# Kernel tuning notes

Hardware: AMD Instinct MI355X
Metric: run time of the kernel (lower is better)

The kernel has to match this reference:

```python
import jax, jax.numpy as jnp
import numpy as np

N_NODES = 50000
N_EDGES = 800000
IN_DIM = 64
OUT_DIM = 64
HID = OUT_DIM // 2  # 32
N_LAYERS = 9  # layer_num; layer_num >= 7 => no temporal conv, conv dropout unused


def _layernorm(x, w, b, eps=1e-5):
    mu = jnp.mean(x, axis=-1, keepdims=True)
    var = jnp.var(x, axis=-1, keepdims=True)
    return (x - mu) * jax.lax.rsqrt(var + eps) * w + b


def _conv(x, Wp, Wn, Ws, src, tgt, pos_m, neg_m):
    # relation-wise gather -> linear -> masked merge -> single scatter_add
    xs = x[src]  # [E, d_in]
    m = jnp.where(pos_m[:, None], xs @ Wp.T, 0.0) + jnp.where(neg_m[:, None], xs @ Wn.T, 0.0)
    agg = jax.ops.segment_sum(m, tgt, num_segments=N_NODES)
    return agg + x @ Ws.T


def _asfr(x, ln_w, ln_b, gw, gb):
    xn = _layernorm(x, ln_w, ln_b)
    w = jax.nn.sigmoid(xn @ gw.T + gb)
    w1 = jnp.where(w > 0.5, 1.0, w)
    w2 = jnp.where(w > 0.5, 0.0, w)
    x1 = w1 * x
    x2 = w2 * x
    h = x.shape[1] // 2
    return jnp.concatenate([x1[:, :h] + x2[:, h:], x1[:, h:] + x2[:, :h]], axis=1)


def setup_inputs() -> dict:
    key = jax.random.key(0)
    ks = jax.random.split(key, 24)
    init_emb = jax.random.normal(ks[0], (N_NODES, IN_DIM), dtype=jnp.float32)
    src = jax.random.randint(ks[1], (N_EDGES,), 0, N_NODES)
    tgt = jax.random.randint(ks[2], (N_EDGES,), 0, N_NODES)
    sign = jnp.where(jax.random.uniform(ks[3], (N_EDGES,)) > 0.5, 1, -1).astype(jnp.int64)
    edge_index_s = jnp.stack([src, tgt, sign], axis=1).astype(jnp.int64)

    def w(k, shape, fan_in):
        return jax.random.normal(k, shape, dtype=jnp.float32) * (1.0 / np.sqrt(fan_in))

    inp = dict(init_emb=init_emb, edge_index_s=edge_index_s)
    # conv1: in 64 -> 32, relations pos/neg + self loop (no bias)
    inp["W1_pos"] = w(ks[4], (HID, IN_DIM), IN_DIM)
    inp["W1_neg"] = w(ks[5], (HID, IN_DIM), IN_DIM)
    inp["W1_self"] = w(ks[6], (HID, IN_DIM), IN_DIM)
    # 8 further convs: 32 -> 32, stacked
    L = N_LAYERS - 1
    inp["Wl_pos"] = w(ks[7], (L, HID, HID), HID)
    inp["Wl_neg"] = w(ks[8], (L, HID, HID), HID)
    inp["Wl_self"] = w(ks[9], (L, HID, HID), HID)
    # ASFR
    inp["asfr_ln_w"] = jnp.ones((HID,), jnp.float32)
    inp["asfr_ln_b"] = jnp.zeros((HID,), jnp.float32)
    inp["asfr_gate_w"] = w(ks[10], (HID, HID), HID)
    inp["asfr_gate_b"] = jnp.zeros((HID,), jnp.float32)
    # projection 32 -> 64
    inp["proj_w"] = w(ks[11], (OUT_DIM, HID), HID)
    inp["proj_b"] = jnp.zeros((OUT_DIM,), jnp.float32)
    # readout MLP: 64 -> 64 -> 64 -> 1, layernorm + relu between
    inp["mlp_w1"] = w(ks[12], (OUT_DIM, OUT_DIM), OUT_DIM)
    inp["mlp_b1"] = jnp.zeros((OUT_DIM,), jnp.float32)
    inp["mlp_ln1_w"] = jnp.ones((OUT_DIM,), jnp.float32)
    inp["mlp_ln1_b"] = jnp.zeros((OUT_DIM,), jnp.float32)
    inp["mlp_w2"] = w(ks[13], (OUT_DIM, OUT_DIM), OUT_DIM)
    inp["mlp_b2"] = jnp.zeros((OUT_DIM,), jnp.float32)
    inp["mlp_ln2_w"] = jnp.ones((OUT_DIM,), jnp.float32)
    inp["mlp_ln2_b"] = jnp.zeros((OUT_DIM,), jnp.float32)
    inp["mlp_w3"] = w(ks[14], (1, OUT_DIM), OUT_DIM)
    inp["mlp_b3"] = jnp.zeros((1,), jnp.float32)
    return inp


def reference(init_emb, edge_index_s, W1_pos, W1_neg, W1_self, Wl_pos, Wl_neg, Wl_self,
              asfr_ln_w, asfr_ln_b, asfr_gate_w, asfr_gate_b, proj_w, proj_b,
              mlp_w1, mlp_b1, mlp_ln1_w, mlp_ln1_b, mlp_w2, mlp_b2,
              mlp_ln2_w, mlp_ln2_b, mlp_w3, mlp_b3):
    src = edge_index_s[:, 0]
    tgt = edge_index_s[:, 1]
    sign = edge_index_s[:, 2]
    pos_m = sign > 0
    neg_m = sign < 0

    z = jax.nn.elu(_conv(init_emb, W1_pos, W1_neg, W1_self, src, tgt, pos_m, neg_m))
    z = _asfr(z, asfr_ln_w, asfr_ln_b, asfr_gate_w, asfr_gate_b)
    for i in range(Wl_pos.shape[0]):
        z_new = jax.nn.elu(_conv(z, Wl_pos[i], Wl_neg[i], Wl_self[i], src, tgt, pos_m, neg_m))
        z = z_new if i == 0 else z_new + 0.1 * z
    z = jax.nn.elu(z @ proj_w.T + proj_b)
    # readout MLP (eval mode: dropout identity)
    h = jax.nn.relu(_layernorm(z @ mlp_w1.T + mlp_b1, mlp_ln1_w, mlp_ln1_b))
    h = jax.nn.relu(_layernorm(h @ mlp_w2.T + mlp_b2, mlp_ln2_w, mlp_ln2_b))
    prob = jax.nn.sigmoid(h @ mlp_w3.T + mlp_b3)
    return (z, prob)
```

## Files before the change

### kernel.cpp

```cpp
#include <hip/hip_runtime.h>
#include <hip/hip_bf16.h>

#define NODES 50000
#define EDGES 800000
#define BSH 8
#define NBUCK 196
#define NBIN_BLOCKS 391

__device__ __forceinline__ float elu1(float x) { return x > 0.f ? x : expm1f(x); }

union F4 { float4 v; float f[4]; };

__global__ __launch_bounds__(256) void k_hist2(const int* __restrict__ ei, int* __restrict__ deg,
                                               int* __restrict__ bucket_cnt) {
  __shared__ int cnt[NBUCK];
  int t = threadIdx.x;
  for (int i = t; i < NBUCK; i += 256) cnt[i] = 0;
  __syncthreads();
  int base = blockIdx.x * 2048;
#pragma unroll
  for (int i = 0; i < 8; i++) {
    int e = base + i * 256 + t;
    if (e < EDGES) {
      int tgt = ei[e * 3 + 1];
      atomicAdd(deg + tgt, 1);
      atomicAdd(&cnt[tgt >> BSH], 1);
    }
  }
  __syncthreads();
  for (int i = t; i < NBUCK; i += 256)
    if (cnt[i]) atomicAdd(bucket_cnt + i, cnt[i]);
}

__global__ __launch_bounds__(512) void k_scan1(const int* __restrict__ deg, int* __restrict__ offs,
                                               int* __restrict__ bsum) {
  __shared__ int s[512];
  int t = threadIdx.x, i = blockIdx.x * 512 + t;
  int v = (i < NODES) ? deg[i] : 0;
  s[t] = v;
  __syncthreads();
  for (int o = 1; o < 512; o <<= 1) {
    int x = (t >= o) ? s[t - o] : 0;
    __syncthreads();
    s[t] += x;
    __syncthreads();
  }
  if (i < NODES) offs[i] = s[t] - v;
  if (t == 511) bsum[blockIdx.x] = s[511];
}

__global__ __launch_bounds__(128) void k_scan2(int* __restrict__ bsum, int nb) {
  __shared__ int s[128];
  int t = threadIdx.x;
  int v = (t < nb) ? bsum[t] : 0;
  s[t] = v;
  __syncthreads();
  for (int o = 1; o < 128; o <<= 1) {
    int x = (t >= o) ? s[t - o] : 0;
    __syncthreads();
    s[t] += x;
    __syncthreads();
  }
  if (t < nb) bsum[t] = s[t] - v;
}

__global__ __launch_bounds__(512) void k_scan3(int* __restrict__ offs, const int* __restrict__ bsum) {
  int i = blockIdx.x * 512 + threadIdx.x;
  if (i < NODES) offs[i] += bsum[blockIdx.x];
  if (i == 0) offs[NODES] = EDGES;
}

__global__ __launch_bounds__(256) void k_bscan(const int* __restrict__ bucket_cnt,
                                               int* __restrict__ bucket_base,
                                               int* __restrict__ bucket_cursor) {
  __shared__ int s[256];
  int t = threadIdx.x;
  int v = (t < NBUCK) ? bucket_cnt[t] : 0;
  s[t] = v;
  __syncthreads();
  for (int o = 1; o < 256; o <<= 1) {
    int x = (t >= o) ? s[t - o] : 0;
    __syncthreads();
    s[t] += x;
    __syncthreads();
  }
  if (t < NBUCK) { int e = s[t] - v; bucket_base[t] = e; bucket_cursor[t] = e; }
}

__global__ __launch_bounds__(256) void k_bin(const int* __restrict__ ei,
                                             int* __restrict__ bucket_cursor,
                                             uint2* __restrict__ binned) {
  __shared__ int cnt[NBUCK], base[NBUCK];
  int t = threadIdx.x;
  for (int i = t; i < NBUCK; i += 256) cnt[i] = 0;
  __syncthreads();
  int eb = blockIdx.x * 2048;
#pragma unroll
  for (int i = 0; i < 8; i++) {
    int e = eb + i * 256 + t;
    if (e < EDGES) atomicAdd(&cnt[ei[e * 3 + 1] >> BSH], 1);
  }
  __syncthreads();
  for (int i = t; i < NBUCK; i += 256) {
    int c = cnt[i];
    base[i] = c ? atomicAdd(bucket_cursor + i, c) : 0;
    cnt[i] = 0;
  }
  __syncthreads();
#pragma unroll
  for (int i = 0; i < 8; i++) {
    int e = eb + i * 256 + t;
    if (e < EDGES) {
      int src = ei[e * 3 + 0];
      int tgt = ei[e * 3 + 1];
      int sg  = ei[e * 3 + 2];
      unsigned val = (unsigned)src | (sg < 0 ? 0x80000000u : 0u);
      int bkt = tgt >> BSH;
      int r = atomicAdd(&cnt[bkt], 1);
      binned[base[bkt] + r] = make_uint2(val, (unsigned)tgt);
    }
  }
}

__global__ __launch_bounds__(256) void k_scatter2(const uint2* __restrict__ binned,
                                                  const int* __restrict__ bucket_base,
                                                  const int* __restrict__ bucket_cnt,
                                                  const int* __restrict__ offs,
                                                  unsigned* __restrict__ perm) {
  __shared__ int cur[256];
  int b = blockIdx.x, t = threadIdx.x;
  int t0 = b << BSH;
  cur[t] = (t0 + t < NODES) ? offs[t0 + t] : 0;
  __syncthreads();
  int n = bucket_cnt[b], bb = bucket_base[b];
  for (int i = t; i < n; i += 256) {
    uint2 e = binned[bb + i];
    int p = atomicAdd(&cur[e.y - t0], 1);
    perm[p] = e.x;
  }
}

__global__ __launch_bounds__(256) void k_lin64(const float* __restrict__ x,
    const float* __restrict__ Wp, const float* __restrict__ Wn, const float* __restrict__ Ws,
    __hip_bfloat16* __restrict__ ypb, __hip_bfloat16* __restrict__ ynb, float* __restrict__ ys) {
  constexpr int K4 = 16;
  __shared__ float4 wp[K4][32], wn[K4][32], wsm[K4][32];
  __shared__ float4 xs[8][K4];
  for (int i = threadIdx.x; i < 32 * K4; i += 256) {
    int k4 = i >> 5, c = i & 31;
    wp[k4][c]  = ((const float4*)Wp)[c * K4 + k4];
    wn[k4][c]  = ((const float4*)Wn)[c * K4 + k4];
    wsm[k4][c] = ((const float4*)Ws)[c * K4 + k4];
  }
  int base = blockIdx.x * 8;
  for (int i = threadIdx.x; i < 8 * K4; i += 256) {
    int r = i / K4, k4 = i - r * K4;
    xs[r][k4] = ((const float4*)(x + (size_t)(base + r) * 64))[k4];
  }
  __syncthreads();
  int lane = threadIdx.x & 31, local = threadIdx.x >> 5;
  float ap = 0.f, an = 0.f, asf = 0.f;
#pragma unroll
  for (int k4 = 0; k4 < K4; k4++) {
    float4 xv = xs[local][k4];
    float4 a = wp[k4][lane], b = wn[k4][lane], c = wsm[k4][lane];
    ap  = fmaf(xv.w, a.w, fmaf(xv.z, a.z, fmaf(xv.y, a.y, fmaf(xv.x, a.x, ap))));
    an  = fmaf(xv.w, b.w, fmaf(xv.z, b.z, fmaf(xv.y, b.y, fmaf(xv.x, b.x, an))));
    asf = fmaf(xv.w, c.w, fmaf(xv.z, c.z, fmaf(xv.y, c.y, fmaf(xv.x, c.x, asf))));
  }
  size_t o = (size_t)(base + local) * 32 + lane;
  ypb[o] = __float2bfloat16(ap);
  ynb[o] = __float2bfloat16(an);
  ys[o] = asf;
}

#define ACC8(A, V)                                   \
  A[0] += __uint_as_float((V).x << 16);              \
  A[1] += __uint_as_float((V).x & 0xffff0000u);      \
  A[2] += __uint_as_float((V).y << 16);              \
  A[3] += __uint_as_float((V).y & 0xffff0000u);      \
  A[4] += __uint_as_float((V).z << 16);              \
  A[5] += __uint_as_float((V).z & 0xffff0000u);      \
  A[6] += __uint_as_float((V).w << 16);              \
  A[7] += __uint_as_float((V).w & 0xffff0000u);

template <int DO_ASFR, int DO_RES, int DO_LIN, int WRITE_Z>
__global__ __launch_bounds__(256) void k_layer(
    const unsigned short* __restrict__ ypi, const unsigned short* __restrict__ yni,
    float* __restrict__ ys,
    const unsigned* __restrict__ perm, const int* __restrict__ offs,
    float* __restrict__ z,
    const float* __restrict__ lnw, const float* __restrict__ lnb,
    const float* __restrict__ gw, const float* __restrict__ gb,
    const float* __restrict__ Wp, const float* __restrict__ Wn, const float* __restrict__ Ws,
    __hip_bfloat16* __restrict__ ypo, __hip_bfloat16* __restrict__ yno) {
  __shared__ float4 wps[8][32], wns[8][32], wss[8][32], gws[8][32];
  __shared__ float zrow[8][36], xrow[8][36];
  int t = threadIdx.x;
  if (DO_LIN) {
    int k4 = t >> 5, c = t & 31;
    wps[k4][c] = ((const float4*)Wp)[c * 8 + k4];
    wns[k4][c] = ((const float4*)Wn)[c * 8 + k4];
    wss[k4][c] = ((const float4*)Ws)[c * 8 + k4];
    if (DO_ASFR) gws[k4][c] = ((const float4*)gw)[c * 8 + k4];
  }
  int lane = t & 31, local = t >> 5;
  int node = blockIdx.x * 8 + local;
  int es = lane >> 2, fs = lane & 3;
  int beg = offs[node], end = offs[node + 1];
  float a0[8], a1[8];
#pragma unroll
  for (int i = 0; i < 8; i++) { a0[i] = 0.f; a1[i] = 0.f; }
  int b = beg + es;
  for (; b + 8 < end; b += 16) {
    unsigned u0 = perm[b];
    unsigned u1 = perm[b + 8];
    const unsigned short* p0 = (u0 >> 31) ? yni : ypi;
    const unsigned short* p1 = (u1 >> 31) ? yni : ypi;
    uint4 v0 = *((const uint4*)(p0 + (size_t)(u0 & 0x7FFFFFFFu) * 32) + fs);
    uint4 v1 = *((const uint4*)(p1 + (size_t)(u1 & 0x7FFFFFFFu) * 32) + fs);
    ACC8(a0, v0);
    ACC8(a1, v1);
  }
  if (b < end) {
    unsigned u0 = perm[b];
    const unsigned short* p0 = (u0 >> 31) ? yni : ypi;
    uint4 v0 = *((const uint4*)(p0 + (size_t)(u0 & 0x7FFFFFFFu) * 32) + fs);
    ACC8(a0, v0);
  }
#pragma unroll
  for (int i = 0; i < 8; i++) a0[i] += a1[i];
#pragma unroll
  for (int m = 4; m <= 16; m <<= 1) {
#pragma unroll
    for (int i = 0; i < 8; i++) a0[i] += __shfl_xor(a0[i], m, 32);
  }
  if (es == 0) {
    const float* ysr = ys + (size_t)node * 32 + fs * 8;
    F4 s0, s1;
    s0.v = *(const float4*)ysr;
    s1.v = *(const float4*)(ysr + 4);
    float o[8];
#pragma unroll
    for (int i = 0; i < 4; i++) o[i] = elu1(a0[i] + s0.f[i]);
#pragma unroll
    for (int i = 0; i < 4; i++) o[4 + i] = elu1(a0[4 + i] + s1.f[i]);
    if (DO_RES) {
      const float* rr = z + (size_t)node * 32 + fs * 8;
      F4 r0, r1;
      r0.v = *(const float4*)rr;
      r1.v = *(const float4*)(rr + 4);
#pragma unroll
      for (int i = 0; i < 4; i++) { o[i] += 0.1f * r0.f[i]; o[4 + i] += 0.1f * r1.f[i]; }
    }
#pragma unroll
    for (int i = 0; i < 8; i++) zrow[local][fs * 8 + i] = o[i];
    if (WRITE_Z) {
      float* zw = z + (size_t)node * 32 + fs * 8;
      *(float4*)zw = make_float4(o[0], o[1], o[2], o[3]);
      *(float4*)(zw + 4) = make_float4(o[4], o[5], o[6], o[7]);
    }
  }
  __syncthreads();
  if (!DO_LIN) return;
  if (DO_ASFR) {
    float v = zrow[local][lane];
    float s = v;
#pragma unroll
    for (int m = 16; m; m >>= 1) s += __shfl_xor(s, m, 32);
    float mu = s * (1.f / 32.f);
    float d = v - mu, sq = d * d;
#pragma unroll
    for (int m = 16; m; m >>= 1) sq += __shfl_xor(sq, m, 32);
    float xn = d * rsqrtf(sq * (1.f / 32.f) + 1e-5f) * lnw[lane] + lnb[lane];
    xrow[local][lane] = xn;
    float ga = gb[lane];
#pragma unroll
    for (int k4 = 0; k4 < 8; k4++) {
      float4 xv = *((const float4*)&xrow[local][0] + k4);
      float4 w = gws[k4][lane];
      ga = fmaf(xv.w, w.w, fmaf(xv.z, w.z, fmaf(xv.y, w.y, fmaf(xv.x, w.x, ga))));
    }
    float g = 1.f / (1.f + __expf(-ga));
    float w1 = g > 0.5f ? 1.f : g;
    float w2 = g > 0.5f ? 0.f : g;
    float zn = w1 * v + __shfl_xor(w2 * v, 16, 32);
    zrow[local][lane] = zn;
  }
  float ap = 0.f, an = 0.f, asf = 0.f;
#pragma unroll
  for (int k4 = 0; k4 < 8; k4++) {
    float4 xv = *((const float4*)&zrow[local][0] + k4);
    float4 a2 = wps[k4][lane], b2 = wns[k4][lane], c2 = wss[k4][lane];
    ap  = fmaf(xv.w, a2.w, fmaf(xv.z, a2.z, fmaf(xv.y, a2.y, fmaf(xv.x, a2.x, ap))));
    an  = fmaf(xv.w, b2.w, fmaf(xv.z, b2.z, fmaf(xv.y, b2.y, fmaf(xv.x, b2.x, an))));
    asf = fmaf(xv.w, c2.w, fmaf(xv.z, c2.z, fmaf(xv.y, c2.y, fmaf(xv.x, c2.x, asf))));
  }
  size_t o = (size_t)node * 32 + lane;
  ypo[o] = __float2bfloat16(ap);
  yno[o] = __float2bfloat16(an);
  ys[o] = asf;
}

__global__ __launch_bounds__(256) void k_mlp(const float* __restrict__ z,
    const float* __restrict__ pw, const float* __restrict__ pb,
    const float* __restrict__ w1, const float* __restrict__ b1,
    const float* __restrict__ l1w, const float* __restrict__ l1b,
    const float* __restrict__ w2, const float* __restrict__ b2,
    const float* __restrict__ l2w, const float* __restrict__ l2b,
    const float* __restrict__ w3, const float* __restrict__ b3,
    float* __restrict__ outz, float* __restrict__ outp) {
  __shared__ float4 pT4[32 * 16];
  __shared__ float4 w1T4[64 * 16], w2T4[64 * 16];
  __shared__ float4 hbuf4[64 * 17];
  __shared__ float pb_s[64], b1_s[64], l1w_s[64], l1b_s[64], b2_s[64], l2w_s[64], l2b_s[64], w3_s[64];
  int t = threadIdx.x;
  for (int i = t; i < 512; i += 256) {
    int k = i >> 4, j4 = i & 15;
    float4 v;
    v.x = pw[(j4 * 4 + 0) * 32 + k]; v.y = pw[(j4 * 4 + 1) * 32 + k];
    v.z = pw[(j4 * 4 + 2) * 32 + k]; v.w = pw[(j4 * 4 + 3) * 32 + k];
    pT4[i] = v;
  }
  for (int i = t; i < 1024; i += 256) {
    int k = i >> 4, j4 = i & 15;
    float4 v, u;
    v.x = w1[(j4 * 4 + 0) * 64 + k]; v.y = w1[(j4 * 4 + 1) * 64 + k];
    v.z = w1[(j4 * 4 + 2) * 64 + k]; v.w = w1[(j4 * 4 + 3) * 64 + k];
    u.x = w2[(j4 * 4 + 0) * 64 + k]; u.y = w2[(j4 * 4 + 1) * 64 + k];
    u.z = w2[(j4 * 4 + 2) * 64 + k]; u.w = w2[(j4 * 4 + 3) * 64 + k];
    w1T4[i] = v; w2T4[i] = u;
  }
  if (t < 64) {
    pb_s[t] = pb[t]; b1_s[t] = b1[t]; l1w_s[t] = l1w[t]; l1b_s[t] = l1b[t];
    b2_s[t] = b2[t]; l2w_s[t] = l2w[t]; l2b_s[t] = l2b[t]; w3_s[t] = w3[t];
  }
  __syncthreads();
  int g = t >> 2, q = t & 3;
  int node = blockIdx.x * 64 + g;
  if (node >= NODES) return;
  float bb3 = b3[0];
  {
    const float4* z4 = (const float4*)(z + (size_t)node * 32);
    hbuf4[g * 17 + q * 2 + 0] = z4[q * 2 + 0];
    hbuf4[g * 17 + q * 2 + 1] = z4[q * 2 + 1];
  }
  float acc[16], h[16];
#pragma unroll
  for (int i = 0; i < 16; i++) acc[i] = pb_s[q * 16 + i];
#pragma unroll 2
  for (int k4 = 0; k4 < 8; k4++) {
    F4 hv; hv.v = hbuf4[g * 17 + k4];
#pragma unroll
    for (int c = 0; c < 4; c++) {
      float hk = hv.f[c];
      const float4* wrow = &pT4[(k4 * 4 + c) * 16 + q * 4];
#pragma unroll
      for (int j4 = 0; j4 < 4; j4++) {
        float4 w = wrow[j4];
        acc[j4 * 4 + 0] = fmaf(hk, w.x, acc[j4 * 4 + 0]);
        acc[j4 * 4 + 1] = fmaf(hk, w.y, acc[j4 * 4 + 1]);
        acc[j4 * 4 + 2] = fmaf(hk, w.z, acc[j4 * 4 + 2]);
        acc[j4 * 4 + 3] = fmaf(hk, w.w, acc[j4 * 4 + 3]);
      }
    }
  }
#pragma unroll
  for (int i = 0; i < 16; i++) h[i] = elu1(acc[i]);
  {
    float4* oz = (float4*)(outz + (size_t)node * 64 + q * 16);
#pragma unroll
    for (int i4 = 0; i4 < 4; i4++)
      oz[i4] = make_float4(h[i4 * 4], h[i4 * 4 + 1], h[i4 * 4 + 2], h[i4 * 4 + 3]);
#pragma unroll
    for (int i4 = 0; i4 < 4; i4++)
      hbuf4[g * 17 + q * 4 + i4] = make_float4(h[i4 * 4], h[i4 * 4 + 1], h[i4 * 4 + 2], h[i4 * 4 + 3]);
  }
#pragma unroll
  for (int i = 0; i < 16; i++) acc[i] = b1_s[q * 16 + i];
#pragma unroll 2
  for (int k4 = 0; k4 < 16; k4++) {
    F4 hv; hv.v = hbuf4[g * 17 + k4];
#pragma unroll
    for (int c = 0; c < 4; c++) {
      float hk = hv.f[c];
      const float4* wrow = &w1T4[(k4 * 4 + c) * 16 + q * 4];
#pragma unroll
      for (int j4 = 0; j4 < 4; j4++) {
        float4 w = wrow[j4];
        acc[j4 * 4 + 0] = fmaf(hk, w.x, acc[j4 * 4 + 0]);
        acc[j4 * 4 + 1] = fmaf(hk, w.y, acc[j4 * 4 + 1]);
        acc[j4 * 4 + 2] = fmaf(hk, w.z, acc[j4 * 4 + 2]);
        acc[j4 * 4 + 3] = fmaf(hk, w.w, acc[j4 * 4 + 3]);
      }
    }
  }
  {
    float s = 0.f;
#pragma unroll
    for (int i = 0; i < 16; i++) s += acc[i];
    s += __shfl_xor(s, 1, 4); s += __shfl_xor(s, 2, 4);
    float mu = s * (1.f / 64.f);
    float vs = 0.f;
#pragma unroll
    for (int i = 0; i < 16; i++) { float dd = acc[i] - mu; vs += dd * dd; }
    vs += __shfl_xor(vs, 1, 4); vs += __shfl_xor(vs, 2, 4);
    float rs = rsqrtf(vs * (1.f / 64.f) + 1e-5f);
#pragma unroll
    for (int i = 0; i < 16; i++)
      h[i] = fmaxf((acc[i] - mu) * rs * l1w_s[q * 16 + i] + l1b_s[q * 16 + i], 0.f);
  }
#pragma unroll
  for (int i4 = 0; i4 < 4; i4++)
    hbuf4[g * 17 + q * 4 + i4] = make_float4(h[i4 * 4], h[i4 * 4 + 1], h[i4 * 4 + 2], h[i4 * 4 + 3]);
#pragma unroll
  for (int i = 0; i < 16; i++) acc[i] = b2_s[q * 16 + i];
#pragma unroll 2
  for (int k4 = 0; k4 < 16; k4++) {
    F4 hv; hv.v = hbuf4[g * 17 + k4];
#pragma unroll
    for (int c = 0; c < 4; c++) {
      float hk = hv.f[c];
      const float4* wrow = &w2T4[(k4 * 4 + c) * 16 + q * 4];
#pragma unroll
      for (int j4 = 0; j4 < 4; j4++) {
        float4 w = wrow[j4];
        acc[j4 * 4 + 0] = fmaf(hk, w.x, acc[j4 * 4 + 0]);
        acc[j4 * 4 + 1] = fmaf(hk, w.y, acc[j4 * 4 + 1]);
        acc[j4 * 4 + 2] = fmaf(hk, w.z, acc[j4 * 4 + 2]);
        acc[j4 * 4 + 3] = fmaf(hk, w.w, acc[j4 * 4 + 3]);
      }
    }
  }
  {
    float s = 0.f;
#pragma unroll
    for (int i = 0; i < 16; i++) s += acc[i];
    s += __shfl_xor(s, 1, 4); s += __shfl_xor(s, 2, 4);
    float mu = s * (1.f / 64.f);
    float vs = 0.f;
#pragma unroll
    for (int i = 0; i < 16; i++) { float dd = acc[i] - mu; vs += dd * dd; }
    vs += __shfl_xor(vs, 1, 4); vs += __shfl_xor(vs, 2, 4);
    float rs = rsqrtf(vs * (1.f / 64.f) + 1e-5f);
    float p = 0.f;
#pragma unroll
    for (int i = 0; i < 16; i++) {
      float hv2 = fmaxf((acc[i] - mu) * rs * l2w_s[q * 16 + i] + l2b_s[q * 16 + i], 0.f);
      p = fmaf(hv2, w3_s[q * 16 + i], p);
    }
    p += __shfl_xor(p, 1, 4); p += __shfl_xor(p, 2, 4);
    if (q == 0) outp[node] = 1.f / (1.f + __expf(-(p + bb3)));
  }
}

extern "C" void kernel_launch(void* const* d_in, const int* in_sizes, int n_in,
                              void* d_out, int out_size, void* d_ws, size_t ws_size,
                              hipStream_t stream) {
  const float* init_emb = (const float*)d_in[0];
  const int*   ei  = (const int*)d_in[1];
  const float* W1p = (const float*)d_in[2];
  const float* W1n = (const float*)d_in[3];
  const float* W1s = (const float*)d_in[4];
  const float* Wlp = (const float*)d_in[5];
  const float* Wln = (const float*)d_in[6];
  const float* Wls = (const float*)d_in[7];
  const float* lnw = (const float*)d_in[8];
  const float* lnb = (const float*)d_in[9];
  const float* gw  = (const float*)d_in[10];
  const float* gb  = (const float*)d_in[11];
  const float* pw  = (const float*)d_in[12];
  const float* pb  = (const float*)d_in[13];
  const float* w1  = (const float*)d_in[14];
  const float* b1  = (const float*)d_in[15];
  const float* l1w = (const float*)d_in[16];
  const float* l1b = (const float*)d_in[17];
  const float* w2  = (const float*)d_in[18];
  const float* b2  = (const float*)d_in[19];
  const float* l2w = (const float*)d_in[20];
  const float* l2b = (const float*)d_in[21];
  const float* w3  = (const float*)d_in[22];
  const float* b3  = (const float*)d_in[23];

  char* ws = (char*)d_ws;
  size_t off = 0;
  auto alloc = [&](size_t b) { void* p = ws + off; off = (off + b + 255) & ~(size_t)255; return p; };
  __hip_bfloat16* ypA = (__hip_bfloat16*)alloc(NODES * 32 * 2);
  __hip_bfloat16* ynA = (__hip_bfloat16*)alloc(NODES * 32 * 2);
  __hip_bfloat16* ypB = (__hip_bfloat16*)alloc(NODES * 32 * 2);
  __hip_bfloat16* ynB = (__hip_bfloat16*)alloc(NODES * 32 * 2);
  float*    ysel   = (float*)alloc(NODES * 32 * 4);
  float*    zbuf   = (float*)alloc(NODES * 32 * 4);
  unsigned* perm   = (unsigned*)alloc(EDGES * 4);
  int*      deg    = (int*)alloc(NODES * 4);
  int*      offs   = (int*)alloc((NODES + 1) * 4);
  int*      bsum   = (int*)alloc(128 * 4);
  int*      bucket_cnt    = (int*)alloc(NBUCK * 4);
  int*      bucket_base   = (int*)alloc(NBUCK * 4);
  int*      bucket_cursor = (int*)alloc(NBUCK * 4);
  uint2*    binned = (uint2*)ypA;

  hipMemsetAsync(deg, 0, NODES * 4, stream);
  hipMemsetAsync(bucket_cnt, 0, NBUCK * 4, stream);
  k_hist2<<<NBIN_BLOCKS, 256, 0, stream>>>(ei, deg, bucket_cnt);
  int nb = (NODES + 511) / 512;
  k_scan1<<<nb, 512, 0, stream>>>(deg, offs, bsum);
  k_scan2<<<1, 128, 0, stream>>>(bsum, nb);
  k_scan3<<<nb, 512, 0, stream>>>(offs, bsum);
  k_bscan<<<1, 256, 0, stream>>>(bucket_cnt, bucket_base, bucket_cursor);
  k_bin<<<NBIN_BLOCKS, 256, 0, stream>>>(ei, bucket_cursor, binned);
  k_scatter2<<<NBUCK, 256, 0, stream>>>(binned, bucket_base, bucket_cnt, offs, perm);

  const int G = NODES / 8;
  k_lin64<<<G, 256, 0, stream>>>(init_emb, W1p, W1n, W1s, ypA, ynA, ysel);
  k_layer<1, 0, 1, 0><<<G, 256, 0, stream>>>((const unsigned short*)ypA, (const unsigned short*)ynA,
      ysel, perm, offs, zbuf, lnw, lnb, gw, gb, Wlp, Wln, Wls, ypB, ynB);
  k_layer<0, 0, 1, 1><<<G, 256, 0, stream>>>((const unsigned short*)ypB, (const unsigned short*)ynB,
      ysel, perm, offs, zbuf, nullptr, nullptr, nullptr, nullptr,
      Wlp + 1024, Wln + 1024, Wls + 1024, ypA, ynA);
  const __hip_bfloat16* yin_p = ypA; const __hip_bfloat16* yin_n = ynA;
  __hip_bfloat16* yout_p = ypB; __hip_bfloat16* yout_n = ynB;
  for (int i = 1; i < 7; i++) {
    k_layer<0, 1, 1, 1><<<G, 256, 0, stream>>>((const unsigned short*)yin_p, (const unsigned short*)yin_n,
        ysel, perm, offs, zbuf, nullptr, nullptr, nullptr, nullptr,
        Wlp + (i + 1) * 1024, Wln + (i + 1) * 1024, Wls + (i + 1) * 1024, yout_p, yout_n);
    const __hip_bfloat16* tp = yin_p; const __hip_bfloat16* tn = yin_n;
    yin_p = yout_p; yin_n = yout_n;
    yout_p = (__hip_bfloat16*)tp; yout_n = (__hip_bfloat16*)tn;
  }
  k_layer<0, 1, 0, 1><<<G, 256, 0, stream>>>((const unsigned short*)yin_p, (const unsigned short*)yin_n,
      ysel, perm, offs, zbuf, nullptr, nullptr, nullptr, nullptr,
      nullptr, nullptr, nullptr, nullptr, nullptr);

  float* outz = (float*)d_out;
  float* outp = outz + (size_t)NODES * 64;
  k_mlp<<<(NODES * 4 + 255) / 256, 256, 0, stream>>>(zbuf, pw, pb, w1, b1, l1w, l1b,
                                                     w2, b2, l2w, l2b, w3, b3, outz, outp);
}
```

Measured before the change: 395.7 us.

## Batch edge index loads via shuffles and shrink MLP smem/registers per node

The layer gather now has each lane load one perm entry per 32-edge chunk and broadcast it with shuffles, which cuts per-lane index loads and raises memory-level parallelism with four accumulator sets. The readout MLP kernel now uses 8 threads per node and 8 outputs each, and reuses one shared weight buffer for w1 and then w2. This lowers shared memory and register use to raise occupancy, at the cost of an extra block barrier and a mid-kernel reload of the w2 weights.

```diff
diff --git a/kernel.cpp b/kernel.cpp
--- a/kernel.cpp
+++ b/kernel.cpp
@@ -208,28 +208,33 @@
   int node = blockIdx.x * 8 + local;
   int es = lane >> 2, fs = lane & 3;
   int beg = offs[node], end = offs[node + 1];
-  float a0[8], a1[8];
-#pragma unroll
-  for (int i = 0; i < 8; i++) { a0[i] = 0.f; a1[i] = 0.f; }
-  int b = beg + es;
-  for (; b + 8 < end; b += 16) {
-    unsigned u0 = perm[b];
-    unsigned u1 = perm[b + 8];
+  float a0[8], a1[8], a2[8], a3[8];
+#pragma unroll
+  for (int i = 0; i < 8; i++) { a0[i] = 0.f; a1[i] = 0.f; a2[i] = 0.f; a3[i] = 0.f; }
+  for (int base = beg; base < end; base += 32) {
+    unsigned pe = (base + lane < end) ? perm[base + lane] : 0u;
+    int rem = end - base;
+    unsigned u0 = __shfl(pe, es, 32);
+    unsigned u1 = __shfl(pe, es + 8, 32);
     const unsigned short* p0 = (u0 >> 31) ? yni : ypi;
     const unsigned short* p1 = (u1 >> 31) ? yni : ypi;
     uint4 v0 = *((const uint4*)(p0 + (size_t)(u0 & 0x7FFFFFFFu) * 32) + fs);
     uint4 v1 = *((const uint4*)(p1 + (size_t)(u1 & 0x7FFFFFFFu) * 32) + fs);
-    ACC8(a0, v0);
-    ACC8(a1, v1);
-  }
-  if (b < end) {
-    unsigned u0 = perm[b];
-    const unsigned short* p0 = (u0 >> 31) ? yni : ypi;
-    uint4 v0 = *((const uint4*)(p0 + (size_t)(u0 & 0x7FFFFFFFu) * 32) + fs);
-    ACC8(a0, v0);
-  }
-#pragma unroll
-  for (int i = 0; i < 8; i++) a0[i] += a1[i];
+    if (es < rem) { ACC8(a0, v0); }
+    if (es + 8 < rem) { ACC8(a1, v1); }
+    if (rem > 16) {
+      unsigned u2 = __shfl(pe, es + 16, 32);
+      unsigned u3 = __shfl(pe, es + 24, 32);
+      const unsigned short* p2 = (u2 >> 31) ? yni : ypi;
+      const unsigned short* p3 = (u3 >> 31) ? yni : ypi;
+      uint4 v2 = *((const uint4*)(p2 + (size_t)(u2 & 0x7FFFFFFFu) * 32) + fs);
+      uint4 v3 = *((const uint4*)(p3 + (size_t)(u3 & 0x7FFFFFFFu) * 32) + fs);
+      if (es + 16 < rem) { ACC8(a2, v2); }
+      if (es + 24 < rem) { ACC8(a3, v3); }
+    }
+  }
+#pragma unroll
+  for (int i = 0; i < 8; i++) a0[i] += (a1[i] + a2[i]) + a3[i];
 #pragma unroll
   for (int m = 4; m <= 16; m <<= 1) {
 #pragma unroll
@@ -291,8 +296,8 @@
 #pragma unroll
   for (int k4 = 0; k4 < 8; k4++) {
     float4 xv = *((const float4*)&zrow[local][0] + k4);
-    float4 a2 = wps[k4][lane], b2 = wns[k4][lane], c2 = wss[k4][lane];
-    ap  = fmaf(xv.w, a2.w, fmaf(xv.z, a2.z, fmaf(xv.y, a2.y, fmaf(xv.x, a2.x, ap))));
+    float4 a2w = wps[k4][lane], b2 = wns[k4][lane], c2 = wss[k4][lane];
+    ap  = fmaf(xv.w, a2w.w, fmaf(xv.z, a2w.z, fmaf(xv.y, a2w.y, fmaf(xv.x, a2w.x, ap))));
     an  = fmaf(xv.w, b2.w, fmaf(xv.z, b2.z, fmaf(xv.y, b2.y, fmaf(xv.x, b2.x, an))));
     asf = fmaf(xv.w, c2.w, fmaf(xv.z, c2.z, fmaf(xv.y, c2.y, fmaf(xv.x, c2.x, asf))));
   }
@@ -310,9 +315,8 @@
     const float* __restrict__ l2w, const float* __restrict__ l2b,
     const float* __restrict__ w3, const float* __restrict__ b3,
     float* __restrict__ outz, float* __restrict__ outp) {
-  __shared__ float4 pT4[32 * 16];
-  __shared__ float4 w1T4[64 * 16], w2T4[64 * 16];
-  __shared__ float4 hbuf4[64 * 17];
+  __shared__ float4 wbuf[1536];
+  __shared__ float4 hbuf4[32 * 17];
   __shared__ float pb_s[64], b1_s[64], l1w_s[64], l1b_s[64], b2_s[64], l2w_s[64], l2b_s[64], w3_s[64];
   int t = threadIdx.x;
   for (int i = t; i < 512; i += 256) {
@@ -320,136 +324,129 @@
     float4 v;
     v.x = pw[(j4 * 4 + 0) * 32 + k]; v.y = pw[(j4 * 4 + 1) * 32 + k];
     v.z = pw[(j4 * 4 + 2) * 32 + k]; v.w = pw[(j4 * 4 + 3) * 32 + k];
-    pT4[i] = v;
+    wbuf[i] = v;
   }
   for (int i = t; i < 1024; i += 256) {
     int k = i >> 4, j4 = i & 15;
-    float4 v, u;
+    float4 v;
     v.x = w1[(j4 * 4 + 0) * 64 + k]; v.y = w1[(j4 * 4 + 1) * 64 + k];
     v.z = w1[(j4 * 4 + 2) * 64 + k]; v.w = w1[(j4 * 4 + 3) * 64 + k];
-    u.x = w2[(j4 * 4 + 0) * 64 + k]; u.y = w2[(j4 * 4 + 1) * 64 + k];
-    u.z = w2[(j4 * 4 + 2) * 64 + k]; u.w = w2[(j4 * 4 + 3) * 64 + k];
-    w1T4[i] = v; w2T4[i] = u;
+    wbuf[512 + i] = v;
   }
   if (t < 64) {
     pb_s[t] = pb[t]; b1_s[t] = b1[t]; l1w_s[t] = l1w[t]; l1b_s[t] = l1b[t];
     b2_s[t] = b2[t]; l2w_s[t] = l2w[t]; l2b_s[t] = l2b[t]; w3_s[t] = w3[t];
   }
   __syncthreads();
-  int g = t >> 2, q = t & 3;
-  int node = blockIdx.x * 64 + g;
-  if (node >= NODES) return;
+  int g = t >> 3, q = t & 7;
+  int node = blockIdx.x * 32 + g;
+  bool live = node < NODES;
   float bb3 = b3[0];
-  {
-    const float4* z4 = (const float4*)(z + (size_t)node * 32);
-    hbuf4[g * 17 + q * 2 + 0] = z4[q * 2 + 0];
-    hbuf4[g * 17 + q * 2 + 1] = z4[q * 2 + 1];
-  }
-  float acc[16], h[16];
-#pragma unroll
-  for (int i = 0; i < 16; i++) acc[i] = pb_s[q * 16 + i];
+  float acc[8], h[8];
+  if (live) {
+    hbuf4[g * 17 + q] = ((const float4*)(z + (size_t)node * 32))[q];
+#pragma unroll
+    for (int i = 0; i < 8; i++) acc[i] = pb_s[q * 8 + i];
 #pragma unroll 2
-  for (int k4 = 0; k4 < 8; k4++) {
-    F4 hv; hv.v = hbuf4[g * 17 + k4];
-#pragma unroll
-    for (int c = 0; c < 4; c++) {
-      float hk = hv.f[c];
-      const float4* wrow = &pT4[(k4 * 4 + c) * 16 + q * 4];
-#pragma unroll
-      for (int j4 = 0; j4 < 4; j4++) {
-        float4 w = wrow[j4];
-        acc[j4 * 4 + 0] = fmaf(hk, w.x, acc[j4 * 4 + 0]);
-        acc[j4 * 4 + 1] = fmaf(hk, w.y, acc[j4 * 4 + 1]);
-        acc[j4 * 4 + 2] = fmaf(hk, w.z, acc[j4 * 4 + 2]);
-        acc[j4 * 4 + 3] = fmaf(hk, w.w, acc[j4 * 4 + 3]);
+    for (int k4 = 0; k4 < 8; k4++) {
+      F4 hv; hv.v = hbuf4[g * 17 + k4];
+#pragma unroll
+      for (int c = 0; c < 4; c++) {
+        float hk = hv.f[c];
+        float4 wa = wbuf[(k4 * 4 + c) * 16 + q * 2];
+        float4 wb = wbuf[(k4 * 4 + c) * 16 + q * 2 + 1];
+        acc[0] = fmaf(hk, wa.x, acc[0]); acc[1] = fmaf(hk, wa.y, acc[1]);
+        acc[2] = fmaf(hk, wa.z, acc[2]); acc[3] = fmaf(hk, wa.w, acc[3]);
+        acc[4] = fmaf(hk, wb.x, acc[4]); acc[5] = fmaf(hk, wb.y, acc[5]);
+        acc[6] = fmaf(hk, wb.z, acc[6]); acc[7] = fmaf(hk, wb.w, acc[7]);
       }
     }
-  }
-#pragma unroll
-  for (int i = 0; i < 16; i++) h[i] = elu1(acc[i]);
-  {
-    float4* oz = (float4*)(outz + (size_t)node * 64 + q * 16);
-#pragma unroll
-    for (int i4 = 0; i4 < 4; i4++)
-      oz[i4] = make_float4(h[i4 * 4], h[i4 * 4 + 1], h[i4 * 4 + 2], h[i4 * 4 + 3]);
-#pragma unroll
-    for (int i4 = 0; i4 < 4; i4++)
-      hbuf4[g * 17 + q * 4 + i4] = make_float4(h[i4 * 4], h[i4 * 4 + 1], h[i4 * 4 + 2], h[i4 * 4 + 3]);
-  }
-#pragma unroll
-  for (int i = 0; i < 16; i++) acc[i] = b1_s[q * 16 + i];
+#pragma unroll
+    for (int i = 0; i < 8; i++) h[i] = elu1(acc[i]);
+    float4 h0 = make_float4(h[0], h[1], h[2], h[3]);
+    float4 h1 = make_float4(h[4], h[5], h[6], h[7]);
+    float4* oz = (float4*)(outz + (size_t)node * 64 + q * 8);
+    oz[0] = h0; oz[1] = h1;
+    hbuf4[g * 17 + 2 * q] = h0;
+    hbuf4[g * 17 + 2 * q + 1] = h1;
+#pragma unroll
+    for (int i = 0; i < 8; i++) acc[i] = b1_s[q * 8 + i];
+#pragma unroll 2
+    for (int k4 = 0; k4 < 16; k4++) {
+      F4 hv; hv.v = hbuf4[g * 17 + k4];
+#pragma unroll
+      for (int c = 0; c < 4; c++) {
+        float hk = hv.f[c];
+        float4 wa = wbuf[512 + (k4 * 4 + c) * 16 + q * 2];
+        float4 wb = wbuf[512 + (k4 * 4 + c) * 16 + q * 2 + 1];
+        acc[0] = fmaf(hk, wa.x, acc[0]); acc[1] = fmaf(hk, wa.y, acc[1]);
+        acc[2] = fmaf(hk, wa.z, acc[2]); acc[3] = fmaf(hk, wa.w, acc[3]);
+        acc[4] = fmaf(hk, wb.x, acc[4]); acc[5] = fmaf(hk, wb.y, acc[5]);
+        acc[6] = fmaf(hk, wb.z, acc[6]); acc[7] = fmaf(hk, wb.w, acc[7]);
+      }
+    }
+  }
+  __syncthreads();
+  for (int i = t; i < 1024; i += 256) {
+    int k = i >> 4, j4 = i & 15;
+    float4 v;
+    v.x = w2[(j4 * 4 + 0) * 64 + k]; v.y = w2[(j4 * 4 + 1) * 64 + k];
+    v.z = w2[(j4 * 4 + 2) * 64 + k]; v.w = w2[(j4 * 4 + 3) * 64 + k];
+    wbuf[i] = v;
+  }
+  if (live) {
+    float s = 0.f;
+#pragma unroll
+    for (int i = 0; i < 8; i++) s += acc[i];
+    s += __shfl_xor(s, 1, 8); s += __shfl_xor(s, 2, 8); s += __shfl_xor(s, 4, 8);
+    float mu = s * (1.f / 64.f);
+    float vs = 0.f;
+#pragma unroll
+    for (int i = 0; i < 8; i++) { float dd = acc[i] - mu; vs += dd * dd; }
+    vs += __shfl_xor(vs, 1, 8); vs += __shfl_xor(vs, 2, 8); vs += __shfl_xor(vs, 4, 8);
+    float rs = rsqrtf(vs * (1.f / 64.f) + 1e-5f);
+#pragma unroll
+    for (int i = 0; i < 8; i++)
+      h[i] = fmaxf((acc[i] - mu) * rs * l1w_s[q * 8 + i] + l1b_s[q * 8 + i], 0.f);
+  }
+  __syncthreads();
+  if (!live) return;
+  hbuf4[g * 17 + 2 * q] = make_float4(h[0], h[1], h[2], h[3]);
+  hbuf4[g * 17 + 2 * q + 1] = make_float4(h[4], h[5], h[6], h[7]);
+#pragma unroll
+  for (int i = 0; i < 8; i++) acc[i] = b2_s[q * 8 + i];
 #pragma unroll 2
   for (int k4 = 0; k4 < 16; k4++) {
     F4 hv; hv.v = hbuf4[g * 17 + k4];
 #pragma unroll
     for (int c = 0; c < 4; c++) {
       float hk = hv.f[c];
-      const float4* wrow = &w1T4[(k4 * 4 + c) * 16 + q * 4];
-#pragma unroll
-      for (int j4 = 0; j4 < 4; j4++) {
-        float4 w = wrow[j4];
-        acc[j4 * 4 + 0] = fmaf(hk, w.x, acc[j4 * 4 + 0]);
-        acc[j4 * 4 + 1] = fmaf(hk, w.y, acc[j4 * 4 + 1]);
-        acc[j4 * 4 + 2] = fmaf(hk, w.z, acc[j4 * 4 + 2]);
-        acc[j4 * 4 + 3] = fmaf(hk, w.w, acc[j4 * 4 + 3]);
-      }
+      float4 wa = wbuf[(k4 * 4 + c) * 16 + q * 2];
+      float4 wb = wbuf[(k4 * 4 + c) * 16 + q * 2 + 1];
+      acc[0] = fmaf(hk, wa.x, acc[0]); acc[1] = fmaf(hk, wa.y, acc[1]);
+      acc[2] = fmaf(hk, wa.z, acc[2]); acc[3] = fmaf(hk, wa.w, acc[3]);
+      acc[4] = fmaf(hk, wb.x, acc[4]); acc[5] = fmaf(hk, wb.y, acc[5]);
+      acc[6] = fmaf(hk, wb.z, acc[6]); acc[7] = fmaf(hk, wb.w, acc[7]);
     }
   }
   {
     float s = 0.f;
 #pragma unroll
-    for (int i = 0; i < 16; i++) s += acc[i];
-    s += __shfl_xor(s, 1, 4); s += __shfl_xor(s, 2, 4);
+    for (int i = 0; i < 8; i++) s += acc[i];
+    s += __shfl_xor(s, 1, 8); s += __shfl_xor(s, 2, 8); s += __shfl_xor(s, 4, 8);
     float mu = s * (1.f / 64.f);
     float vs = 0.f;
 #pragma unroll
-    for (int i = 0; i < 16; i++) { float dd = acc[i] - mu; vs += dd * dd; }
-    vs += __shfl_xor(vs, 1, 4); vs += __shfl_xor(vs, 2, 4);
-    float rs = rsqrtf(vs * (1.f / 64.f) + 1e-5f);
-#pragma unroll
-    for (int i = 0; i < 16; i++)
-      h[i] = fmaxf((acc[i] - mu) * rs * l1w_s[q * 16 + i] + l1b_s[q * 16 + i], 0.f);
-  }
-#pragma unroll
-  for (int i4 = 0; i4 < 4; i4++)
-    hbuf4[g * 17 + q * 4 + i4] = make_float4(h[i4 * 4], h[i4 * 4 + 1], h[i4 * 4 + 2], h[i4 * 4 + 3]);
-#pragma unroll
-  for (int i = 0; i < 16; i++) acc[i] = b2_s[q * 16 + i];
-#pragma unroll 2
-  for (int k4 = 0; k4 < 16; k4++) {
-    F4 hv; hv.v = hbuf4[g * 17 + k4];
-#pragma unroll
-    for (int c = 0; c < 4; c++) {
-      float hk = hv.f[c];
-      const float4* wrow = &w2T4[(k4 * 4 + c) * 16 + q * 4];
-#pragma unroll
-      for (int j4 = 0; j4 < 4; j4++) {
-        float4 w = wrow[j4];
-        acc[j4 * 4 + 0] = fmaf(hk, w.x, acc[j4 * 4 + 0]);
-        acc[j4 * 4 + 1] = fmaf(hk, w.y, acc[j4 * 4 + 1]);
-        acc[j4 * 4 + 2] = fmaf(hk, w.z, acc[j4 * 4 + 2]);
-        acc[j4 * 4 + 3] = fmaf(hk, w.w, acc[j4 * 4 + 3]);
-      }
-    }
-  }
-  {
-    float s = 0.f;
-#pragma unroll
-    for (int i = 0; i < 16; i++) s += acc[i];
-    s += __shfl_xor(s, 1, 4); s += __shfl_xor(s, 2, 4);
-    float mu = s * (1.f / 64.f);
-    float vs = 0.f;
-#pragma unroll
-    for (int i = 0; i < 16; i++) { float dd = acc[i] - mu; vs += dd * dd; }
-    vs += __shfl_xor(vs, 1, 4); vs += __shfl_xor(vs, 2, 4);
+    for (int i = 0; i < 8; i++) { float dd = acc[i] - mu; vs += dd * dd; }
+    vs += __shfl_xor(vs, 1, 8); vs += __shfl_xor(vs, 2, 8); vs += __shfl_xor(vs, 4, 8);
     float rs = rsqrtf(vs * (1.f / 64.f) + 1e-5f);
     float p = 0.f;
 #pragma unroll
-    for (int i = 0; i < 16; i++) {
-      float hv2 = fmaxf((acc[i] - mu) * rs * l2w_s[q * 16 + i] + l2b_s[q * 16 + i], 0.f);
-      p = fmaf(hv2, w3_s[q * 16 + i], p);
-    }
-    p += __shfl_xor(p, 1, 4); p += __shfl_xor(p, 2, 4);
+    for (int i = 0; i < 8; i++) {
+      float hv2 = fmaxf((acc[i] - mu) * rs * l2w_s[q * 8 + i] + l2b_s[q * 8 + i], 0.f);
+      p = fmaf(hv2, w3_s[q * 8 + i], p);
+    }
+    p += __shfl_xor(p, 1, 8); p += __shfl_xor(p, 2, 8); p += __shfl_xor(p, 4, 8);
     if (q == 0) outp[node] = 1.f / (1.f + __expf(-(p + bb3)));
   }
 }
@@ -534,6 +531,6 @@
 
   float* outz = (float*)d_out;
   float* outp = outz + (size_t)NODES * 64;
-  k_mlp<<<(NODES * 4 + 255) / 256, 256, 0, stream>>>(zbuf, pw, pb, w1, b1, l1w, l1b,
-                                                     w2, b2, l2w, l2b, w3, b3, outz, outp);
-}
+  k_mlp<<<(NODES + 31) / 32, 256, 0, stream>>>(zbuf, pw, pb, w1, b1, l1w, l1b,
+                                               w2, b2, l2w, l2b, w3, b3, outz, outp);
+}
```

After: 395.0 us. Within noise of the previous version (-0.2%).
